# Kernel tuning notes

Measured on AMD Instinct MI355X. Metric: run time of the kernel, lower is better.

The kernel has to match this reference:

```python
import jax, jax.numpy as jnp
import numpy as np

N = 8192      # num nodes
D = 256       # input feature dim (num_embeddings)
F_OUT = 128   # out_channels
B = 4096      # lookup batch size


def setup_inputs() -> dict:
    key = jax.random.key(0)
    k1, k2, k3, k4 = jax.random.split(key, 4)
    x = jax.random.randint(k1, (B,), 0, N)                      # node ids for final lookup
    adj = jax.random.randint(k2, (N, N), 0, 2).astype(jnp.int32)  # dense 0/1 adjacency
    embedding = jax.random.normal(k3, (N, D), dtype=jnp.float32)
    xavier = 1.414 * (6.0 / (D + F_OUT)) ** 0.5
    W = jax.random.uniform(k4, (D, F_OUT), minval=-xavier, maxval=xavier, dtype=jnp.float32)
    return {"x": x, "adj": adj, "embedding": embedding, "W": W}


def reference(x, adj, embedding, W):
    Wh = embedding @ W                                   # [N, F_OUT]
    mask = adj > 0
    maskf = mask.astype(Wh.dtype)
    # per-row neighbor mean of Wh (vectorized form of the python row loop)
    deg = jnp.maximum(jnp.sum(maskf, axis=1), 1.0)       # guard; random adj has deg>0
    neigh_mean = (maskf @ Wh) / deg[:, None]             # [N, F_OUT]
    alpha = jnp.sum(Wh * neigh_mean, axis=1)             # [N], Wh[i] . mean(neighbors)
    e = Wh @ Wh.T + alpha[:, None]                       # similarity + row-wise query term
    att = jax.nn.softmax(jnp.where(mask, e, jnp.asarray(-9e15, e.dtype)), axis=1)
    # dropout is identity in eval mode (p effectively 0)
    h_prime = att @ Wh                                   # [N, F_OUT]
    emb_out = jax.nn.elu(h_prime)                        # concat=True branch
    out = emb_out[x]                                     # F.embedding lookup, [B, F_OUT]
    nrm = jnp.linalg.norm(out, axis=1, keepdims=True)
    return out / jnp.maximum(nrm, 1e-12)                 # F.normalize (L2, eps=1e-12)
```

## Files before the change

### kernel.cpp

```cpp
#include <hip/hip_runtime.h>

#define NN 8192
#define DD 256
#define FF 128
#define BB 4096
#define NSPLIT 16
#define KCHUNK (NN / NSPLIT)
#define NITER (KCHUNK / 64)

typedef unsigned short ushortT;
typedef __attribute__((ext_vector_type(8))) short bf16x8;
typedef __attribute__((ext_vector_type(4))) float f32x4;

__device__ __forceinline__ ushortT f2bf(float f) {
  unsigned u = __float_as_uint(f);
  return (ushortT)((u + 0x7FFFu + ((u >> 16) & 1u)) >> 16);
}
__device__ __forceinline__ float bf2f(ushortT h) {
  return __uint_as_float(((unsigned)h) << 16);
}


__global__ __launch_bounds__(256) void init_kernel(int* flags, int* cnt) {
  int i = blockIdx.x * 256 + threadIdx.x;
  flags[i] = 0;
  if (i == 0) *cnt = 0;
}

__global__ __launch_bounds__(256) void scatter_kernel(const int* __restrict__ x, int* flags) {
  int b = blockIdx.x * 256 + threadIdx.x;
  flags[x[b]] = 1;
}

__global__ __launch_bounds__(256) void compact_kernel(const int* __restrict__ flags, int* cnt,
                                                      int* list, int* slot) {
  int i = blockIdx.x * 256 + threadIdx.x;
  if (flags[i]) {
    int pos = atomicAdd(cnt, 1);
    list[pos] = i;
    slot[i] = pos;
  }
}


__global__ __launch_bounds__(256) void pack_kernel(const int* __restrict__ adj,
                                                   const int* __restrict__ list,
                                                   const int* __restrict__ cntp,
                                                   unsigned* __restrict__ pk) {
  const int s = blockIdx.x >> 2;
  const int kc = (blockIdx.x & 3) * 2048;
  if (s >= *cntp) return;
  const int w = threadIdx.x >> 6, l = threadIdx.x & 63;
  const int* base = adj + (size_t)list[s] * NN + kc + w * 512;
  unsigned long long* dst = (unsigned long long*)(pk + s * 256 + (kc >> 5) + w * 16);
#pragma unroll
  for (int i = 0; i < 8; ++i) {
    unsigned long long b = __ballot(base[i * 64 + l] > 0);
    if (l == 0) dst[i] = b;
  }
}


__global__ __launch_bounds__(256) void wh_kernel(const float* __restrict__ emb,
                                                 const float* __restrict__ W,
                                                 ushortT* __restrict__ Whh,
                                                 ushortT* __restrict__ Whl) {
  __shared__ float Es[32 * 65];
  __shared__ float Ws[64 * 128];
  const int t = threadIdx.x;
  const int r0 = blockIdx.x * 32;
  const int rg = t >> 5;
  const int cg = t & 31;
  float4 acc[4] = {{0,0,0,0},{0,0,0,0},{0,0,0,0},{0,0,0,0}};
  for (int kc = 0; kc < DD; kc += 64) {
    __syncthreads();
    for (int i = 0; i < 8; ++i) {
      int idx = t + 256 * i;
      int r = idx >> 6, k = idx & 63;
      Es[r * 65 + k] = emb[(r0 + r) * DD + kc + k];
    }
    for (int i = 0; i < 8; ++i) {
      int idx = t + 256 * i;
      int kr = idx >> 5, c4 = (idx & 31) * 4;
      *(float4*)&Ws[kr * 128 + c4] = *(const float4*)&W[(kc + kr) * 128 + c4];
    }
    __syncthreads();
    for (int k = 0; k < 64; ++k) {
      float4 b = *(const float4*)&Ws[k * 128 + cg * 4];
#pragma unroll
      for (int i = 0; i < 4; ++i) {
        float a = Es[(rg * 4 + i) * 65 + k];
        acc[i].x += a * b.x; acc[i].y += a * b.y;
        acc[i].z += a * b.z; acc[i].w += a * b.w;
      }
    }
  }
#pragma unroll
  for (int i = 0; i < 4; ++i) {
    int row = r0 + rg * 4 + i;
    float v[4] = {acc[i].x, acc[i].y, acc[i].z, acc[i].w};
    ushort4 hh, ll;
    ushortT* hp = (ushortT*)&hh;
    ushortT* lp = (ushortT*)&ll;
#pragma unroll
    for (int k = 0; k < 4; ++k) {
      ushortT h = f2bf(v[k]);
      hp[k] = h;
      lp[k] = f2bf(v[k] - bf2f(h));
    }
    *(ushort4*)&Whh[row * FF + cg * 4] = hh;
    *(ushort4*)&Whl[row * FF + cg * 4] = ll;
  }
}


__global__ __launch_bounds__(256) void transpose_kernel(const ushortT* __restrict__ A,
                                                        ushortT* __restrict__ At) {
  __shared__ ushortT tile[64 * 72];
  const int t = threadIdx.x;
  const int r0 = (blockIdx.x >> 1) * 64, c0 = (blockIdx.x & 1) * 64;
#pragma unroll
  for (int i = 0; i < 2; ++i) {
    int idx = t + 256 * i;
    int r = idx >> 3, cb = idx & 7;
    *(bf16x8*)&tile[r * 72 + ((cb ^ ((r >> 3) & 7)) * 8)] =
        *(const bf16x8*)&A[(size_t)(r0 + r) * FF + c0 + cb * 8];
  }
  __syncthreads();
#pragma unroll
  for (int i = 0; i < 2; ++i) {
    int idx = t + 256 * i;
    int f = idx >> 3, r8 = idx & 7;
    bf16x8 v;
#pragma unroll
    for (int u = 0; u < 8; ++u) {
      int row = r8 * 8 + u;
      v[u] = (short)tile[row * 72 + (((f >> 3) ^ ((row >> 3) & 7)) * 8) + (f & 7)];
    }
    *(bf16x8*)&At[(size_t)(c0 + f) * NN + r0 + r8 * 8] = v;
  }
}


__global__ __launch_bounds__(256, 2) void attn_kernel(
    const ushortT* __restrict__ Whh, const ushortT* __restrict__ Whl,
    const ushortT* __restrict__ WhT, const unsigned* __restrict__ pk,
    const int* __restrict__ list, const int* __restrict__ cntp,
    float* __restrict__ Opart, float* __restrict__ mpart, float* __restrict__ lpart) {
  __shared__ short Kh[64 * 128];
  __shared__ short Kl[64 * 128];
  __shared__ short Vs[128 * 64];
  __shared__ short Ps[4][16 * 72];
  __shared__ int nid[64];

  const int cnt = *cntp;
  const int qblk = blockIdx.x >> 4, chunk = blockIdx.x & 15;
  const int q0 = qblk * 64;
  if (q0 >= cnt) return;

  const int t = threadIdx.x;
  if (t < 64) nid[t] = list[min(q0 + t, cnt - 1)];
  __syncthreads();

  const int w = t >> 6, l = t & 63, quad = l >> 4, c = l & 15;

  const size_t qr = (size_t)nid[w * 16 + c] * FF;
  bf16x8 qh[4], ql[4];
#pragma unroll
  for (int ks = 0; ks < 4; ++ks) {
    qh[ks] = *(const bf16x8*)(Whh + qr + ks * 32 + quad * 8);
    ql[ks] = *(const bf16x8*)(Whl + qr + ks * 32 + quad * 8);
  }
  int prow[4];
#pragma unroll
  for (int r = 0; r < 4; ++r) prow[r] = min(q0 + w * 16 + quad * 4 + r, cnt - 1);

  float m[4], lr[4];
#pragma unroll
  for (int r = 0; r < 4; ++r) { m[r] = -1e30f; lr[r] = 0.f; }
  f32x4 O[8] = {{0,0,0,0},{0,0,0,0},{0,0,0,0},{0,0,0,0},
                {0,0,0,0},{0,0,0,0},{0,0,0,0},{0,0,0,0}};

  const int kt0 = chunk * KCHUNK;

  bf16x8 sgh[4], sgl[4], sgv[4];
  {
    const ushortT* gh = Whh + (size_t)kt0 * FF;
    const ushortT* gl = Whl + (size_t)kt0 * FF;
#pragma unroll
    for (int i = 0; i < 4; ++i) {
      int idx = t + 256 * i;
      sgh[i] = *(const bf16x8*)(gh + idx * 8);
      sgl[i] = *(const bf16x8*)(gl + idx * 8);
      int vr = idx >> 3, vcb = idx & 7;
      sgv[i] = *(const bf16x8*)(WhT + (size_t)vr * NN + kt0 + vcb * 8);
    }
#pragma unroll
    for (int i = 0; i < 4; ++i) {
      int idx = t + 256 * i;
      int r = idx >> 4, cb = idx & 15;
      int off = r * 128 + ((cb ^ (r & 7)) * 8);
      *(bf16x8*)&Kh[off] = sgh[i];
      *(bf16x8*)&Kl[off] = sgl[i];
      int vr = idx >> 3, vcb = idx & 7;
      *(bf16x8*)&Vs[vr * 64 + ((vcb ^ (vr & 7)) * 8)] = sgv[i];
    }
  }
  __syncthreads();

  for (int it = 0; it < NITER; ++it) {
    const int kt = kt0 + it * 64;

    if (it + 1 < NITER) {
      const ushortT* gh = Whh + (size_t)(kt + 64) * FF;
      const ushortT* gl = Whl + (size_t)(kt + 64) * FF;
#pragma unroll
      for (int i = 0; i < 4; ++i) {
        int idx = t + 256 * i;
        sgh[i] = *(const bf16x8*)(gh + idx * 8);
        sgl[i] = *(const bf16x8*)(gl + idx * 8);
        int vr = idx >> 3, vcb = idx & 7;
        sgv[i] = *(const bf16x8*)(WhT + (size_t)vr * NN + (kt + 64) + vcb * 8);
      }
    }

    unsigned mw0[4], mw1[4];
#pragma unroll
    for (int r = 0; r < 4; ++r) {
      uint2 mm = *(const uint2*)(pk + (size_t)prow[r] * 256 + (kt >> 5));
      mw0[r] = mm.x; mw1[r] = mm.y;
    }

    f32x4 sacc[4];
#pragma unroll
    for (int nt = 0; nt < 4; ++nt) {
      const int rb = (nt * 16 + c) * 128;
      f32x4 a = {0, 0, 0, 0};
#pragma unroll
      for (int ks = 0; ks < 4; ++ks) {
        const int off = rb + (((ks * 4 + quad) ^ (c & 7)) * 8);
        bf16x8 bh = *(const bf16x8*)&Kh[off];
        bf16x8 bl = *(const bf16x8*)&Kl[off];
        a = __builtin_amdgcn_mfma_f32_16x16x32_bf16(qh[ks], bh, a, 0, 0, 0);
        a = __builtin_amdgcn_mfma_f32_16x16x32_bf16(ql[ks], bh, a, 0, 0, 0);
        a = __builtin_amdgcn_mfma_f32_16x16x32_bf16(qh[ks], bl, a, 0, 0, 0);
      }
      sacc[nt] = a;
    }

    float rmax[4];
#pragma unroll
    for (int r = 0; r < 4; ++r) {
      float v = -1e30f;
#pragma unroll
      for (int nt = 0; nt < 4; ++nt) {
        unsigned bit = ((nt < 2 ? mw0[r] : mw1[r]) >> ((nt & 1) * 16 + c)) & 1u;
        v = fmaxf(v, bit ? sacc[nt][r] : -1e30f);
      }
      rmax[r] = v;
    }
#pragma unroll
    for (int mk = 1; mk <= 8; mk <<= 1)
#pragma unroll
      for (int r = 0; r < 4; ++r) rmax[r] = fmaxf(rmax[r], __shfl_xor(rmax[r], mk, 16));
    float sc[4], psum[4];
#pragma unroll
    for (int r = 0; r < 4; ++r) {
      float nm = fmaxf(m[r], rmax[r]);
      sc[r] = __expf(m[r] - nm);
      m[r] = nm;
      psum[r] = 0.f;
    }
#pragma unroll
    for (int nt = 0; nt < 4; ++nt)
#pragma unroll
      for (int r = 0; r < 4; ++r) {
        unsigned bit = ((nt < 2 ? mw0[r] : mw1[r]) >> ((nt & 1) * 16 + c)) & 1u;
        float p = bit ? __expf(sacc[nt][r] - m[r]) : 0.f;
        ushortT pb = f2bf(p);
        Ps[w][(quad * 4 + r) * 72 + nt * 16 + c] = (short)pb;
        psum[r] += bf2f(pb);
      }
#pragma unroll
    for (int mk = 1; mk <= 8; mk <<= 1)
#pragma unroll
      for (int r = 0; r < 4; ++r) psum[r] += __shfl_xor(psum[r], mk, 16);
#pragma unroll
    for (int r = 0; r < 4; ++r) lr[r] = lr[r] * sc[r] + psum[r];

#pragma unroll
    for (int ft = 0; ft < 8; ++ft)
#pragma unroll
      for (int r = 0; r < 4; ++r) O[ft][r] *= sc[r];
    bf16x8 pa[2];
#pragma unroll
    for (int ks2 = 0; ks2 < 2; ++ks2)
      pa[ks2] = *(const bf16x8*)&Ps[w][c * 72 + ks2 * 32 + quad * 8];
#pragma unroll
    for (int ft = 0; ft < 8; ++ft) {
      const int vrow = ft * 16 + c;
#pragma unroll
      for (int ks2 = 0; ks2 < 2; ++ks2) {
        const int voff = vrow * 64 + (((ks2 * 4 + quad) ^ (c & 7)) * 8);
        bf16x8 vb = *(const bf16x8*)&Vs[voff];
        O[ft] = __builtin_amdgcn_mfma_f32_16x16x32_bf16(pa[ks2], vb, O[ft], 0, 0, 0);
      }
    }

    if (it + 1 < NITER) {
      __syncthreads();
#pragma unroll
      for (int i = 0; i < 4; ++i) {
        int idx = t + 256 * i;
        int r = idx >> 4, cb = idx & 15;
        int off = r * 128 + ((cb ^ (r & 7)) * 8);
        *(bf16x8*)&Kh[off] = sgh[i];
        *(bf16x8*)&Kl[off] = sgl[i];
        int vr = idx >> 3, vcb = idx & 7;
        *(bf16x8*)&Vs[vr * 64 + ((vcb ^ (vr & 7)) * 8)] = sgv[i];
      }
      __syncthreads();
    }
  }

  float* Op = Opart + (size_t)chunk * 4096 * FF;
#pragma unroll
  for (int ft = 0; ft < 8; ++ft)
#pragma unroll
    for (int r = 0; r < 4; ++r)
      Op[(size_t)(q0 + w * 16 + quad * 4 + r) * FF + ft * 16 + c] = O[ft][r];
  if (c == 0) {
#pragma unroll
    for (int r = 0; r < 4; ++r) {
      mpart[chunk * 4096 + q0 + w * 16 + quad * 4 + r] = m[r];
      lpart[chunk * 4096 + q0 + w * 16 + quad * 4 + r] = lr[r];
    }
  }
}


__global__ __launch_bounds__(128) void combine_kernel(
    const float* __restrict__ Opart, const float* __restrict__ mpart,
    const float* __restrict__ lpart, float* __restrict__ h) {
  const int r = blockIdx.x;
  const int t = threadIdx.x;
  float mstar = -1e30f;
#pragma unroll
  for (int c = 0; c < NSPLIT; ++c) mstar = fmaxf(mstar, mpart[c * 4096 + r]);
  float lstar = 0.f, acc = 0.f;
#pragma unroll
  for (int c = 0; c < NSPLIT; ++c) {
    float wgt = __expf(mpart[c * 4096 + r] - mstar);
    lstar += wgt * lpart[c * 4096 + r];
    acc += wgt * Opart[((size_t)c * 4096 + r) * FF + t];
  }
  float v = acc / fmaxf(lstar, 1e-30f);
  h[r * FF + t] = v > 0.f ? v : expm1f(v);
}


__global__ __launch_bounds__(128) void out_kernel(const int* __restrict__ x,
                                                  const int* __restrict__ slot,
                                                  const float* __restrict__ h,
                                                  float* __restrict__ out) {
  const int b = blockIdx.x, t = threadIdx.x;
  const int s = slot[x[b]];
  float v = h[s * FF + t];
  float ss = v * v;
#pragma unroll
  for (int wd = 1; wd <= 32; wd <<= 1) ss += __shfl_xor(ss, wd);
  __shared__ float red[2];
  if ((t & 63) == 0) red[t >> 6] = ss;
  __syncthreads();
  float tot = red[0] + red[1];
  float scale = 1.f / fmaxf(sqrtf(tot), 1e-12f);
  out[b * FF + t] = v * scale;
}


extern "C" void kernel_launch(void* const* d_in, const int* in_sizes, int n_in,
                              void* d_out, int out_size, void* d_ws, size_t ws_size,
                              hipStream_t stream) {
  const int*   x   = (const int*)d_in[0];
  const int*   adj = (const int*)d_in[1];
  const float* emb = (const float*)d_in[2];
  const float* W   = (const float*)d_in[3];
  float* out = (float*)d_out;

  char* base = (char*)d_ws;
  ushortT* Whh = (ushortT*)(base);
  ushortT* Whl = (ushortT*)(base + 2097152);
  float*   h   = (float*)(base + 2097152);
  ushortT* WhT = (ushortT*)(base + 4194304);
  float* Opart = (float*)(base + 6291456);
  float* mpart = (float*)(base + 39845888);
  float* lpart = (float*)(base + 40108032);
  unsigned* pk = (unsigned*)(base + 40370176);
  int*   flags = (int*)(base + 44564480);
  int*   list  = (int*)(base + 44597248);
  int*   slot  = (int*)(base + 44613632);
  int*   cnt   = (int*)(base + 44646400);
  (void)in_sizes; (void)n_in; (void)out_size; (void)ws_size;

  hipLaunchKernelGGL(init_kernel,      dim3(NN / 256), dim3(256), 0, stream, flags, cnt);
  hipLaunchKernelGGL(scatter_kernel,   dim3(BB / 256), dim3(256), 0, stream, x, flags);
  hipLaunchKernelGGL(compact_kernel,   dim3(NN / 256), dim3(256), 0, stream, flags, cnt, list, slot);
  hipLaunchKernelGGL(pack_kernel,      dim3(4096 * 4), dim3(256), 0, stream, adj, list, cnt, pk);
  hipLaunchKernelGGL(wh_kernel,        dim3(NN / 32),  dim3(256), 0, stream, emb, W, Whh, Whl);
  hipLaunchKernelGGL(transpose_kernel, dim3((NN / 64) * 2), dim3(256), 0, stream, Whh, WhT);
  hipLaunchKernelGGL(attn_kernel,      dim3((BB / 64) * NSPLIT), dim3(256), 0, stream,
                     Whh, Whl, WhT, pk, list, cnt, Opart, mpart, lpart);
  hipLaunchKernelGGL(combine_kernel,   dim3(4096), dim3(128), 0, stream, Opart, mpart, lpart, h);
  hipLaunchKernelGGL(out_kernel,       dim3(BB),   dim3(128), 0, stream, x, slot, h, out);
}
```

Before: 439.4 us.

## Switch attention to 32x32 MFMA with 128-query blocks and register-resident P

Rewrites the attention inner loop to use 32x32x16 bf16 MFMA, computing S transposed so each lane owns a full query row. The softmax max and sum reductions shrink to a single cross-half shuffle. P is repacked into MFMA operands through lane shuffles instead of an LDS round trip. Query blocks double to 128 rows and the key range is split 19 ways with uneven tile ranges, which balances the grid across CUs but adds register pressure and a more complex combine.

New measurement: 435.0 us. No clear change (-1.0%).

```diff
diff --git a/kernel.cpp b/kernel.cpp
--- a/kernel.cpp
+++ b/kernel.cpp
@@ -4,13 +4,13 @@
 #define DD 256
 #define FF 128
 #define BB 4096
-#define NSPLIT 16
-#define KCHUNK (NN / NSPLIT)
-#define NITER (KCHUNK / 64)
+#define NSPLIT 19
+#define NTILES 128
 
 typedef unsigned short ushortT;
 typedef __attribute__((ext_vector_type(8))) short bf16x8;
 typedef __attribute__((ext_vector_type(4))) float f32x4;
+typedef __attribute__((ext_vector_type(16))) float f32x16;
 
 __device__ __forceinline__ ushortT f2bf(float f) {
   unsigned u = __float_as_uint(f);
@@ -150,41 +150,41 @@
   __shared__ short Kh[64 * 128];
   __shared__ short Kl[64 * 128];
   __shared__ short Vs[128 * 64];
-  __shared__ short Ps[4][16 * 72];
-  __shared__ int nid[64];
+  __shared__ int nid[128];
 
   const int cnt = *cntp;
-  const int qblk = blockIdx.x >> 4, chunk = blockIdx.x & 15;
-  const int q0 = qblk * 64;
+  const int qblk = blockIdx.x / NSPLIT, chunk = blockIdx.x % NSPLIT;
+  const int q0 = qblk * 128;
   if (q0 >= cnt) return;
 
   const int t = threadIdx.x;
-  if (t < 64) nid[t] = list[min(q0 + t, cnt - 1)];
+  if (t < 128) nid[t] = list[min(q0 + t, cnt - 1)];
   __syncthreads();
 
-  const int w = t >> 6, l = t & 63, quad = l >> 4, c = l & 15;
-
-  const size_t qr = (size_t)nid[w * 16 + c] * FF;
-  bf16x8 qh[4], ql[4];
-#pragma unroll
-  for (int ks = 0; ks < 4; ++ks) {
-    qh[ks] = *(const bf16x8*)(Whh + qr + ks * 32 + quad * 8);
-    ql[ks] = *(const bf16x8*)(Whl + qr + ks * 32 + quad * 8);
-  }
-  int prow[4];
-#pragma unroll
-  for (int r = 0; r < 4; ++r) prow[r] = min(q0 + w * 16 + quad * 4 + r, cnt - 1);
-
-  float m[4], lr[4];
-#pragma unroll
-  for (int r = 0; r < 4; ++r) { m[r] = -1e30f; lr[r] = 0.f; }
-  f32x4 O[8] = {{0,0,0,0},{0,0,0,0},{0,0,0,0},{0,0,0,0},
-                {0,0,0,0},{0,0,0,0},{0,0,0,0},{0,0,0,0}};
-
-  const int kt0 = chunk * KCHUNK;
+  const int w = t >> 6, l = t & 63, h = l >> 5, lq = l & 31;
+
+  const size_t qr = (size_t)nid[w * 32 + lq] * FF;
+  bf16x8 qh[8], ql[8];
+#pragma unroll
+  for (int st = 0; st < 8; ++st) {
+    qh[st] = *(const bf16x8*)(Whh + qr + st * 16 + h * 8);
+    ql[st] = *(const bf16x8*)(Whl + qr + st * 16 + h * 8);
+  }
+  const int prow = min(q0 + w * 32 + lq, cnt - 1);
+
+  float m = -1e30f, lr = 0.f;
+  f32x16 O[4];
+#pragma unroll
+  for (int ft = 0; ft < 4; ++ft)
+#pragma unroll
+    for (int e = 0; e < 16; ++e) O[ft][e] = 0.f;
+
+  const int ts = (chunk * NTILES) / NSPLIT;
+  const int te = ((chunk + 1) * NTILES) / NSPLIT;
 
   bf16x8 sgh[4], sgl[4], sgv[4];
   {
+    const int kt0 = ts * 64;
     const ushortT* gh = Whh + (size_t)kt0 * FF;
     const ushortT* gl = Whl + (size_t)kt0 * FF;
 #pragma unroll
@@ -208,10 +208,10 @@
   }
   __syncthreads();
 
-  for (int it = 0; it < NITER; ++it) {
-    const int kt = kt0 + it * 64;
-
-    if (it + 1 < NITER) {
+  for (int it = ts; it < te; ++it) {
+    const int kt = it * 64;
+
+    if (it + 1 < te) {
       const ushortT* gh = Whh + (size_t)(kt + 64) * FF;
       const ushortT* gl = Whl + (size_t)(kt + 64) * FF;
 #pragma unroll
@@ -224,90 +224,94 @@
       }
     }
 
-    unsigned mw0[4], mw1[4];
-#pragma unroll
-    for (int r = 0; r < 4; ++r) {
-      uint2 mm = *(const uint2*)(pk + (size_t)prow[r] * 256 + (kt >> 5));
-      mw0[r] = mm.x; mw1[r] = mm.y;
-    }
-
-    f32x4 sacc[4];
-#pragma unroll
-    for (int nt = 0; nt < 4; ++nt) {
-      const int rb = (nt * 16 + c) * 128;
-      f32x4 a = {0, 0, 0, 0};
-#pragma unroll
-      for (int ks = 0; ks < 4; ++ks) {
-        const int off = rb + (((ks * 4 + quad) ^ (c & 7)) * 8);
-        bf16x8 bh = *(const bf16x8*)&Kh[off];
-        bf16x8 bl = *(const bf16x8*)&Kl[off];
-        a = __builtin_amdgcn_mfma_f32_16x16x32_bf16(qh[ks], bh, a, 0, 0, 0);
-        a = __builtin_amdgcn_mfma_f32_16x16x32_bf16(ql[ks], bh, a, 0, 0, 0);
-        a = __builtin_amdgcn_mfma_f32_16x16x32_bf16(qh[ks], bl, a, 0, 0, 0);
+    const uint2 mm = *(const uint2*)(pk + (size_t)prow * 256 + (kt >> 5));
+
+    f32x16 s0, s1;
+#pragma unroll
+    for (int e = 0; e < 16; ++e) { s0[e] = 0.f; s1[e] = 0.f; }
+#pragma unroll
+    for (int st = 0; st < 8; ++st) {
+      const int cb = st * 2 + h;
+      const int o0 = lq * 128 + ((cb ^ (lq & 7)) * 8);
+      bf16x8 ah = *(const bf16x8*)&Kh[o0];
+      bf16x8 al = *(const bf16x8*)&Kl[o0];
+      s0 = __builtin_amdgcn_mfma_f32_32x32x16_bf16(ah, qh[st], s0, 0, 0, 0);
+      s0 = __builtin_amdgcn_mfma_f32_32x32x16_bf16(ah, ql[st], s0, 0, 0, 0);
+      s0 = __builtin_amdgcn_mfma_f32_32x32x16_bf16(al, qh[st], s0, 0, 0, 0);
+      const int r1 = 32 + lq;
+      const int o1 = r1 * 128 + ((cb ^ (r1 & 7)) * 8);
+      bf16x8 bh = *(const bf16x8*)&Kh[o1];
+      bf16x8 bl = *(const bf16x8*)&Kl[o1];
+      s1 = __builtin_amdgcn_mfma_f32_32x32x16_bf16(bh, qh[st], s1, 0, 0, 0);
+      s1 = __builtin_amdgcn_mfma_f32_32x32x16_bf16(bh, ql[st], s1, 0, 0, 0);
+      s1 = __builtin_amdgcn_mfma_f32_32x32x16_bf16(bl, qh[st], s1, 0, 0, 0);
+    }
+
+    float rmx = -1e30f;
+#pragma unroll
+    for (int rg = 0; rg < 16; ++rg) {
+      const int sh = (rg & 3) + 8 * (rg >> 2) + 4 * h;
+      rmx = fmaxf(rmx, ((mm.x >> sh) & 1u) ? s0[rg] : -1e30f);
+      rmx = fmaxf(rmx, ((mm.y >> sh) & 1u) ? s1[rg] : -1e30f);
+    }
+    rmx = fmaxf(rmx, __shfl_xor(rmx, 32));
+    const float nm = fmaxf(m, rmx);
+    const float sc = __expf(m - nm);
+    m = nm;
+    float psum = 0.f;
+    unsigned pw[16];
+#pragma unroll
+    for (int kk = 0; kk < 8; ++kk) {
+      const int rgA = 2 * kk, rgB = 2 * kk + 1;
+      const int shA = (rgA & 3) + 8 * (rgA >> 2) + 4 * h;
+      const int shB = (rgB & 3) + 8 * (rgB >> 2) + 4 * h;
+      float pA0 = ((mm.x >> shA) & 1u) ? __expf(s0[rgA] - m) : 0.f;
+      float pB0 = ((mm.x >> shB) & 1u) ? __expf(s0[rgB] - m) : 0.f;
+      ushortT qA0 = f2bf(pA0), qB0 = f2bf(pB0);
+      psum += bf2f(qA0); psum += bf2f(qB0);
+      pw[kk] = (unsigned)qA0 | ((unsigned)qB0 << 16);
+      float pA1 = ((mm.y >> shA) & 1u) ? __expf(s1[rgA] - m) : 0.f;
+      float pB1 = ((mm.y >> shB) & 1u) ? __expf(s1[rgB] - m) : 0.f;
+      ushortT qA1 = f2bf(pA1), qB1 = f2bf(pB1);
+      psum += bf2f(qA1); psum += bf2f(qB1);
+      pw[8 + kk] = (unsigned)qA1 | ((unsigned)qB1 << 16);
+    }
+    psum += __shfl_xor(psum, 32);
+    lr = lr * sc + psum;
+
+    bf16x8 pa[4];
+#pragma unroll
+    for (int s = 0; s < 4; ++s) {
+      const unsigned g0 = pw[4 * s], g1 = pw[4 * s + 1];
+      const unsigned g2 = pw[4 * s + 2], g3 = pw[4 * s + 3];
+      const unsigned k0 = h ? g2 : g0, k1 = h ? g3 : g1;
+      const unsigned x0 = h ? g0 : g2, x1 = h ? g1 : g3;
+      const unsigned r0 = (unsigned)__shfl_xor((int)x0, 32);
+      const unsigned r1 = (unsigned)__shfl_xor((int)x1, 32);
+      union { unsigned u[4]; bf16x8 v; } uu;
+      uu.u[0] = h ? r0 : k0;
+      uu.u[1] = h ? r1 : k1;
+      uu.u[2] = h ? k0 : r0;
+      uu.u[3] = h ? k1 : r1;
+      pa[s] = uu.v;
+    }
+
+#pragma unroll
+    for (int ft = 0; ft < 4; ++ft)
+#pragma unroll
+      for (int e = 0; e < 16; ++e) O[ft][e] *= sc;
+#pragma unroll
+    for (int ft = 0; ft < 4; ++ft) {
+      const int vr = ft * 32 + lq;
+#pragma unroll
+      for (int st = 0; st < 4; ++st) {
+        const int cb = st * 2 + h;
+        bf16x8 vb = *(const bf16x8*)&Vs[vr * 64 + ((cb ^ (vr & 7)) * 8)];
+        O[ft] = __builtin_amdgcn_mfma_f32_32x32x16_bf16(vb, pa[st], O[ft], 0, 0, 0);
       }
-      sacc[nt] = a;
-    }
-
-    float rmax[4];
-#pragma unroll
-    for (int r = 0; r < 4; ++r) {
-      float v = -1e30f;
-#pragma unroll
-      for (int nt = 0; nt < 4; ++nt) {
-        unsigned bit = ((nt < 2 ? mw0[r] : mw1[r]) >> ((nt & 1) * 16 + c)) & 1u;
-        v = fmaxf(v, bit ? sacc[nt][r] : -1e30f);
-      }
-      rmax[r] = v;
-    }
-#pragma unroll
-    for (int mk = 1; mk <= 8; mk <<= 1)
-#pragma unroll
-      for (int r = 0; r < 4; ++r) rmax[r] = fmaxf(rmax[r], __shfl_xor(rmax[r], mk, 16));
-    float sc[4], psum[4];
-#pragma unroll
-    for (int r = 0; r < 4; ++r) {
-      float nm = fmaxf(m[r], rmax[r]);
-      sc[r] = __expf(m[r] - nm);
-      m[r] = nm;
-      psum[r] = 0.f;
-    }
-#pragma unroll
-    for (int nt = 0; nt < 4; ++nt)
-#pragma unroll
-      for (int r = 0; r < 4; ++r) {
-        unsigned bit = ((nt < 2 ? mw0[r] : mw1[r]) >> ((nt & 1) * 16 + c)) & 1u;
-        float p = bit ? __expf(sacc[nt][r] - m[r]) : 0.f;
-        ushortT pb = f2bf(p);
-        Ps[w][(quad * 4 + r) * 72 + nt * 16 + c] = (short)pb;
-        psum[r] += bf2f(pb);
-      }
-#pragma unroll
-    for (int mk = 1; mk <= 8; mk <<= 1)
-#pragma unroll
-      for (int r = 0; r < 4; ++r) psum[r] += __shfl_xor(psum[r], mk, 16);
-#pragma unroll
-    for (int r = 0; r < 4; ++r) lr[r] = lr[r] * sc[r] + psum[r];
-
-#pragma unroll
-    for (int ft = 0; ft < 8; ++ft)
-#pragma unroll
-      for (int r = 0; r < 4; ++r) O[ft][r] *= sc[r];
-    bf16x8 pa[2];
-#pragma unroll
-    for (int ks2 = 0; ks2 < 2; ++ks2)
-      pa[ks2] = *(const bf16x8*)&Ps[w][c * 72 + ks2 * 32 + quad * 8];
-#pragma unroll
-    for (int ft = 0; ft < 8; ++ft) {
-      const int vrow = ft * 16 + c;
-#pragma unroll
-      for (int ks2 = 0; ks2 < 2; ++ks2) {
-        const int voff = vrow * 64 + (((ks2 * 4 + quad) ^ (c & 7)) * 8);
-        bf16x8 vb = *(const bf16x8*)&Vs[voff];
-        O[ft] = __builtin_amdgcn_mfma_f32_16x16x32_bf16(pa[ks2], vb, O[ft], 0, 0, 0);
-      }
-    }
-
-    if (it + 1 < NITER) {
+    }
+
+    if (it + 1 < te) {
       __syncthreads();
 #pragma unroll
       for (int i = 0; i < 4; ++i) {
@@ -324,17 +328,17 @@
   }
 
   float* Op = Opart + (size_t)chunk * 4096 * FF;
-#pragma unroll
-  for (int ft = 0; ft < 8; ++ft)
-#pragma unroll
-    for (int r = 0; r < 4; ++r)
-      Op[(size_t)(q0 + w * 16 + quad * 4 + r) * FF + ft * 16 + c] = O[ft][r];
-  if (c == 0) {
-#pragma unroll
-    for (int r = 0; r < 4; ++r) {
-      mpart[chunk * 4096 + q0 + w * 16 + quad * 4 + r] = m[r];
-      lpart[chunk * 4096 + q0 + w * 16 + quad * 4 + r] = lr[r];
-    }
+  const int qrow = q0 + w * 32 + lq;
+#pragma unroll
+  for (int ft = 0; ft < 4; ++ft)
+#pragma unroll
+    for (int a = 0; a < 4; ++a) {
+      float4 v4 = {O[ft][4 * a], O[ft][4 * a + 1], O[ft][4 * a + 2], O[ft][4 * a + 3]};
+      *(float4*)&Op[(size_t)qrow * FF + ft * 32 + a * 8 + h * 4] = v4;
+    }
+  if (h == 0) {
+    mpart[chunk * 4096 + qrow] = m;
+    lpart[chunk * 4096 + qrow] = lr;
   }
 }
 
@@ -393,13 +397,13 @@
   float*   h   = (float*)(base + 2097152);
   ushortT* WhT = (ushortT*)(base + 4194304);
   float* Opart = (float*)(base + 6291456);
-  float* mpart = (float*)(base + 39845888);
-  float* lpart = (float*)(base + 40108032);
-  unsigned* pk = (unsigned*)(base + 40370176);
-  int*   flags = (int*)(base + 44564480);
-  int*   list  = (int*)(base + 44597248);
-  int*   slot  = (int*)(base + 44613632);
-  int*   cnt   = (int*)(base + 44646400);
+  float* mpart = (float*)(base + 46137344);
+  float* lpart = (float*)(base + 46448640);
+  unsigned* pk = (unsigned*)(base + 46759936);
+  int*   flags = (int*)(base + 50954240);
+  int*   list  = (int*)(base + 50987008);
+  int*   slot  = (int*)(base + 51019776);
+  int*   cnt   = (int*)(base + 51052544);
   (void)in_sizes; (void)n_in; (void)out_size; (void)ws_size;
 
   hipLaunchKernelGGL(init_kernel,      dim3(NN / 256), dim3(256), 0, stream, flags, cnt);
@@ -408,7 +412,7 @@
   hipLaunchKernelGGL(pack_kernel,      dim3(4096 * 4), dim3(256), 0, stream, adj, list, cnt, pk);
   hipLaunchKernelGGL(wh_kernel,        dim3(NN / 32),  dim3(256), 0, stream, emb, W, Whh, Whl);
   hipLaunchKernelGGL(transpose_kernel, dim3((NN / 64) * 2), dim3(256), 0, stream, Whh, WhT);
-  hipLaunchKernelGGL(attn_kernel,      dim3((BB / 64) * NSPLIT), dim3(256), 0, stream,
+  hipLaunchKernelGGL(attn_kernel,      dim3((BB / 128) * NSPLIT), dim3(256), 0, stream,
                      Whh, Whl, WhT, pk, list, cnt, Opart, mpart, lpart);
   hipLaunchKernelGGL(combine_kernel,   dim3(4096), dim3(128), 0, stream, Opart, mpart, lpart, h);
   hipLaunchKernelGGL(out_kernel,       dim3(BB),   dim3(128), 0, stream, x, slot, h, out);
```

## Transpose score MFMA so each lane owns one query row, drop P shared buffer

Applied to the files above, without the earlier changes.

Swaps the MFMA operand order so each lane holds a full column of scores for one query row. The row max and sum then need only two cross-lane shuffles instead of a 16-lane reduction over four rows. The P tile is passed to the PV MFMA through register shuffles rather than a shared-memory round trip, which frees LDS and allows launch bounds of 3 blocks per SM. NSPLIT changes from 16 to 15 with uneven tile ranges, likely to match the CU count, and the output writes become float4 stores. The risks are extra register pressure from the shuffles and load imbalance across the uneven chunks.

After: 452.1 us. 2.9% more time.

```diff
diff --git a/kernel.cpp b/kernel.cpp
--- a/kernel.cpp
+++ b/kernel.cpp
@@ -4,9 +4,8 @@
 #define DD 256
 #define FF 128
 #define BB 4096
-#define NSPLIT 16
-#define KCHUNK (NN / NSPLIT)
-#define NITER (KCHUNK / 64)
+#define NSPLIT 15
+#define NTILES 128
 
 typedef unsigned short ushortT;
 typedef __attribute__((ext_vector_type(8))) short bf16x8;
@@ -142,7 +141,7 @@
 }
 
 
-__global__ __launch_bounds__(256, 2) void attn_kernel(
+__global__ __launch_bounds__(256, 3) void attn_kernel(
     const ushortT* __restrict__ Whh, const ushortT* __restrict__ Whl,
     const ushortT* __restrict__ WhT, const unsigned* __restrict__ pk,
     const int* __restrict__ list, const int* __restrict__ cntp,
@@ -150,11 +149,10 @@
   __shared__ short Kh[64 * 128];
   __shared__ short Kl[64 * 128];
   __shared__ short Vs[128 * 64];
-  __shared__ short Ps[4][16 * 72];
   __shared__ int nid[64];
 
   const int cnt = *cntp;
-  const int qblk = blockIdx.x >> 4, chunk = blockIdx.x & 15;
+  const int qblk = blockIdx.x / NSPLIT, chunk = blockIdx.x % NSPLIT;
   const int q0 = qblk * 64;
   if (q0 >= cnt) return;
 
@@ -171,20 +169,18 @@
     qh[ks] = *(const bf16x8*)(Whh + qr + ks * 32 + quad * 8);
     ql[ks] = *(const bf16x8*)(Whl + qr + ks * 32 + quad * 8);
   }
-  int prow[4];
-#pragma unroll
-  for (int r = 0; r < 4; ++r) prow[r] = min(q0 + w * 16 + quad * 4 + r, cnt - 1);
-
-  float m[4], lr[4];
-#pragma unroll
-  for (int r = 0; r < 4; ++r) { m[r] = -1e30f; lr[r] = 0.f; }
+  const int prow = min(q0 + w * 16 + c, cnt - 1);
+
+  float m = -1e30f, lr = 0.f;
   f32x4 O[8] = {{0,0,0,0},{0,0,0,0},{0,0,0,0},{0,0,0,0},
                 {0,0,0,0},{0,0,0,0},{0,0,0,0},{0,0,0,0}};
 
-  const int kt0 = chunk * KCHUNK;
+  const int ts = (chunk * NTILES) / NSPLIT;
+  const int te = ((chunk + 1) * NTILES) / NSPLIT;
 
   bf16x8 sgh[4], sgl[4], sgv[4];
   {
+    const int kt0 = ts * 64;
     const ushortT* gh = Whh + (size_t)kt0 * FF;
     const ushortT* gl = Whl + (size_t)kt0 * FF;
 #pragma unroll
@@ -208,10 +204,10 @@
   }
   __syncthreads();
 
-  for (int it = 0; it < NITER; ++it) {
-    const int kt = kt0 + it * 64;
-
-    if (it + 1 < NITER) {
+  for (int it = ts; it < te; ++it) {
+    const int kt = it * 64;
+
+    if (it + 1 < te) {
       const ushortT* gh = Whh + (size_t)(kt + 64) * FF;
       const ushortT* gl = Whl + (size_t)(kt + 64) * FF;
 #pragma unroll
@@ -224,12 +220,7 @@
       }
     }
 
-    unsigned mw0[4], mw1[4];
-#pragma unroll
-    for (int r = 0; r < 4; ++r) {
-      uint2 mm = *(const uint2*)(pk + (size_t)prow[r] * 256 + (kt >> 5));
-      mw0[r] = mm.x; mw1[r] = mm.y;
-    }
+    const uint2 mm = *(const uint2*)(pk + (size_t)prow * 256 + (kt >> 5));
 
     f32x4 sacc[4];
 #pragma unroll
@@ -239,63 +230,70 @@
 #pragma unroll
       for (int ks = 0; ks < 4; ++ks) {
         const int off = rb + (((ks * 4 + quad) ^ (c & 7)) * 8);
-        bf16x8 bh = *(const bf16x8*)&Kh[off];
-        bf16x8 bl = *(const bf16x8*)&Kl[off];
-        a = __builtin_amdgcn_mfma_f32_16x16x32_bf16(qh[ks], bh, a, 0, 0, 0);
-        a = __builtin_amdgcn_mfma_f32_16x16x32_bf16(ql[ks], bh, a, 0, 0, 0);
-        a = __builtin_amdgcn_mfma_f32_16x16x32_bf16(qh[ks], bl, a, 0, 0, 0);
+        bf16x8 kh = *(const bf16x8*)&Kh[off];
+        bf16x8 kl = *(const bf16x8*)&Kl[off];
+        a = __builtin_amdgcn_mfma_f32_16x16x32_bf16(kh, qh[ks], a, 0, 0, 0);
+        a = __builtin_amdgcn_mfma_f32_16x16x32_bf16(kh, ql[ks], a, 0, 0, 0);
+        a = __builtin_amdgcn_mfma_f32_16x16x32_bf16(kl, qh[ks], a, 0, 0, 0);
       }
       sacc[nt] = a;
     }
 
-    float rmax[4];
-#pragma unroll
-    for (int r = 0; r < 4; ++r) {
-      float v = -1e30f;
-#pragma unroll
-      for (int nt = 0; nt < 4; ++nt) {
-        unsigned bit = ((nt < 2 ? mw0[r] : mw1[r]) >> ((nt & 1) * 16 + c)) & 1u;
-        v = fmaxf(v, bit ? sacc[nt][r] : -1e30f);
-      }
-      rmax[r] = v;
-    }
-#pragma unroll
-    for (int mk = 1; mk <= 8; mk <<= 1)
-#pragma unroll
-      for (int r = 0; r < 4; ++r) rmax[r] = fmaxf(rmax[r], __shfl_xor(rmax[r], mk, 16));
-    float sc[4], psum[4];
-#pragma unroll
-    for (int r = 0; r < 4; ++r) {
-      float nm = fmaxf(m[r], rmax[r]);
-      sc[r] = __expf(m[r] - nm);
-      m[r] = nm;
-      psum[r] = 0.f;
-    }
+    float rmx = -1e30f;
 #pragma unroll
     for (int nt = 0; nt < 4; ++nt)
 #pragma unroll
       for (int r = 0; r < 4; ++r) {
-        unsigned bit = ((nt < 2 ? mw0[r] : mw1[r]) >> ((nt & 1) * 16 + c)) & 1u;
-        float p = bit ? __expf(sacc[nt][r] - m[r]) : 0.f;
-        ushortT pb = f2bf(p);
-        Ps[w][(quad * 4 + r) * 72 + nt * 16 + c] = (short)pb;
-        psum[r] += bf2f(pb);
-      }
-#pragma unroll
-    for (int mk = 1; mk <= 8; mk <<= 1)
-#pragma unroll
-      for (int r = 0; r < 4; ++r) psum[r] += __shfl_xor(psum[r], mk, 16);
-#pragma unroll
-    for (int r = 0; r < 4; ++r) lr[r] = lr[r] * sc[r] + psum[r];
+        const int sh = (nt * 16 + quad * 4 + r) & 31;
+        unsigned bit = ((nt < 2 ? mm.x : mm.y) >> sh) & 1u;
+        rmx = fmaxf(rmx, bit ? sacc[nt][r] : -1e30f);
+      }
+    rmx = fmaxf(rmx, __shfl_xor(rmx, 16));
+    rmx = fmaxf(rmx, __shfl_xor(rmx, 32));
+    const float nm = fmaxf(m, rmx);
+    const float sc = __expf(m - nm);
+    m = nm;
+    float psum = 0.f;
+    unsigned pq[4][2];
+#pragma unroll
+    for (int nt = 0; nt < 4; ++nt)
+#pragma unroll
+      for (int wd = 0; wd < 2; ++wd) {
+        const int r0i = 2 * wd, r1i = 2 * wd + 1;
+        const int sh0 = (nt * 16 + quad * 4 + r0i) & 31;
+        const int sh1 = (nt * 16 + quad * 4 + r1i) & 31;
+        const unsigned mw = (nt < 2 ? mm.x : mm.y);
+        float p0 = ((mw >> sh0) & 1u) ? __expf(sacc[nt][r0i] - m) : 0.f;
+        float p1 = ((mw >> sh1) & 1u) ? __expf(sacc[nt][r1i] - m) : 0.f;
+        ushortT b0 = f2bf(p0), b1 = f2bf(p1);
+        psum += bf2f(b0); psum += bf2f(b1);
+        pq[nt][wd] = (unsigned)b0 | ((unsigned)b1 << 16);
+      }
+    psum += __shfl_xor(psum, 16);
+    psum += __shfl_xor(psum, 32);
+    lr = lr * sc + psum;
+
+    bf16x8 pa[2];
+#pragma unroll
+    for (int ks2 = 0; ks2 < 2; ++ks2) {
+      unsigned res[4];
+      const int srcBase = (2 * (quad & 1)) * 16 + c;
+#pragma unroll
+      for (int u = 0; u < 4; ++u) {
+        const int src = srcBase + (u >> 1) * 16;
+        unsigned lo = (unsigned)__shfl((int)pq[2 * ks2][u & 1], src);
+        unsigned hi = (unsigned)__shfl((int)pq[2 * ks2 + 1][u & 1], src);
+        res[u] = (quad >> 1) ? hi : lo;
+      }
+      union { unsigned u[4]; bf16x8 v; } uu;
+      uu.u[0] = res[0]; uu.u[1] = res[1]; uu.u[2] = res[2]; uu.u[3] = res[3];
+      pa[ks2] = uu.v;
+    }
 
 #pragma unroll
     for (int ft = 0; ft < 8; ++ft)
 #pragma unroll
-      for (int r = 0; r < 4; ++r) O[ft][r] *= sc[r];
-    bf16x8 pa[2];
-#pragma unroll
-    for (int ks2 = 0; ks2 < 2; ++ks2)
-      pa[ks2] = *(const bf16x8*)&Ps[w][c * 72 + ks2 * 32 + quad * 8];
+      for (int r = 0; r < 4; ++r) O[ft][r] *= sc;
 #pragma unroll
     for (int ft = 0; ft < 8; ++ft) {
       const int vrow = ft * 16 + c;
@@ -303,11 +301,11 @@
       for (int ks2 = 0; ks2 < 2; ++ks2) {
         const int voff = vrow * 64 + (((ks2 * 4 + quad) ^ (c & 7)) * 8);
         bf16x8 vb = *(const bf16x8*)&Vs[voff];
-        O[ft] = __builtin_amdgcn_mfma_f32_16x16x32_bf16(pa[ks2], vb, O[ft], 0, 0, 0);
-      }
-    }
-
-    if (it + 1 < NITER) {
+        O[ft] = __builtin_amdgcn_mfma_f32_16x16x32_bf16(vb, pa[ks2], O[ft], 0, 0, 0);
+      }
+    }
+
+    if (it + 1 < te) {
       __syncthreads();
 #pragma unroll
       for (int i = 0; i < 4; ++i) {
@@ -324,17 +322,15 @@
   }
 
   float* Op = Opart + (size_t)chunk * 4096 * FF;
-#pragma unroll
-  for (int ft = 0; ft < 8; ++ft)
-#pragma unroll
-    for (int r = 0; r < 4; ++r)
-      Op[(size_t)(q0 + w * 16 + quad * 4 + r) * FF + ft * 16 + c] = O[ft][r];
-  if (c == 0) {
-#pragma unroll
-    for (int r = 0; r < 4; ++r) {
-      mpart[chunk * 4096 + q0 + w * 16 + quad * 4 + r] = m[r];
-      lpart[chunk * 4096 + q0 + w * 16 + quad * 4 + r] = lr[r];
-    }
+  const int qrow = q0 + w * 16 + c;
+#pragma unroll
+  for (int ft = 0; ft < 8; ++ft) {
+    float4 v4 = {O[ft][0], O[ft][1], O[ft][2], O[ft][3]};
+    *(float4*)&Op[(size_t)qrow * FF + ft * 16 + quad * 4] = v4;
+  }
+  if (quad == 0) {
+    mpart[chunk * 4096 + qrow] = m;
+    lpart[chunk * 4096 + qrow] = lr;
   }
 }
 
@@ -393,13 +389,13 @@
   float*   h   = (float*)(base + 2097152);
   ushortT* WhT = (ushortT*)(base + 4194304);
   float* Opart = (float*)(base + 6291456);
-  float* mpart = (float*)(base + 39845888);
-  float* lpart = (float*)(base + 40108032);
-  unsigned* pk = (unsigned*)(base + 40370176);
-  int*   flags = (int*)(base + 44564480);
-  int*   list  = (int*)(base + 44597248);
-  int*   slot  = (int*)(base + 44613632);
-  int*   cnt   = (int*)(base + 44646400);
+  float* mpart = (float*)(base + 37748736);
+  float* lpart = (float*)(base + 37994496);
+  unsigned* pk = (unsigned*)(base + 38240256);
+  int*   flags = (int*)(base + 42434560);
+  int*   list  = (int*)(base + 42467328);
+  int*   slot  = (int*)(base + 42500096);
+  int*   cnt   = (int*)(base + 42532864);
   (void)in_sizes; (void)n_in; (void)out_size; (void)ws_size;
 
   hipLaunchKernelGGL(init_kernel,      dim3(NN / 256), dim3(256), 0, stream, flags, cnt);
```
